# Kernel optimization log

Hardware: AMD Instinct MI355X
Metric: run time of the kernel (lower is better)

Reference implementation:

```python
import jax, jax.numpy as jnp
import numpy as np

B, S, DIM, H, DH, FF = 2, 2048, 2048, 16, 128, 8192
EPS = 1e-6


def rmsnorm(x, g):
    xf = x.astype(jnp.float32)
    y = xf * jax.lax.rsqrt(jnp.mean(xf * xf, axis=-1, keepdims=True) + EPS)
    return y.astype(x.dtype) * g


def rope_cache(seq_len, head_dim):
    inv_freq = 1.0 / (10000.0 ** (jnp.arange(0, head_dim, 2, dtype=jnp.float32) / head_dim))
    t = jnp.arange(seq_len, dtype=jnp.float32)
    freqs = jnp.outer(t, inv_freq)              # [S, DH/2]
    emb = jnp.concatenate([freqs, freqs], -1)   # [S, DH]
    return jnp.cos(emb), jnp.sin(emb)


def rotate_half(x):
    x1, x2 = jnp.split(x, 2, axis=-1)
    return jnp.concatenate([-x2, x1], axis=-1)


def apply_rope(x, cos, sin):
    # x: [B,H,S,DH]; cos/sin: [S,DH] broadcast per position
    c = cos[None, None, :, :]
    s = sin[None, None, :, :]
    return x * c + rotate_half(x) * s


def setup_inputs() -> dict:
    key = jax.random.key(0)
    ks = jax.random.split(key, 10)
    std = 0.02
    x = jax.random.normal(ks[0], (B, S, DIM), jnp.float32)
    mask = jnp.tril(jnp.ones((S, S), dtype=bool))[None, None]  # causal [1,1,S,S]
    wq = jax.random.normal(ks[1], (H * DH, DIM), jnp.float32) * std
    wk = jax.random.normal(ks[2], (H * DH, DIM), jnp.float32) * std
    wv = jax.random.normal(ks[3], (H * DH, DIM), jnp.float32) * std
    wo = jax.random.normal(ks[4], (DIM, H * DH), jnp.float32) * std
    w1 = jax.random.normal(ks[5], (FF, DIM), jnp.float32) * std
    w2 = jax.random.normal(ks[6], (DIM, FF), jnp.float32) * std
    w3 = jax.random.normal(ks[7], (FF, DIM), jnp.float32) * std
    g_attn = jnp.ones((DIM,), jnp.float32)
    g_ffn = jnp.ones((DIM,), jnp.float32)
    return {"x": x, "mask": mask, "wq": wq, "wk": wk, "wv": wv, "wo": wo,
            "w1": w1, "w2": w2, "w3": w3, "g_attn": g_attn, "g_ffn": g_ffn}


def reference(x, mask, wq, wk, wv, wo, w1, w2, w3, g_attn, g_ffn):
    b, s, _ = x.shape
    scale = 1.0 / np.sqrt(DH)
    # --- attention sublayer ---
    h = rmsnorm(x, g_attn)
    q = jnp.einsum('bsd,ed->bse', h, wq).reshape(b, s, H, DH).transpose(0, 2, 1, 3)
    k = jnp.einsum('bsd,ed->bse', h, wk).reshape(b, s, H, DH).transpose(0, 2, 1, 3)
    v = jnp.einsum('bsd,ed->bse', h, wv).reshape(b, s, H, DH).transpose(0, 2, 1, 3)
    cos, sin = rope_cache(s, DH)
    q = apply_rope(q, cos, sin)
    k = apply_rope(k, cos, sin)
    scores = jnp.einsum('bhqd,bhkd->bhqk', q, k) * scale
    scores = jnp.where(mask, scores, -1e9)
    attn = jax.nn.softmax(scores, axis=-1)
    o = jnp.einsum('bhqk,bhkd->bhqd', attn, v)
    o = o.transpose(0, 2, 1, 3).reshape(b, s, H * DH)
    x = x + jnp.einsum('bse,de->bsd', o, wo)
    # --- SwiGLU FFN sublayer ---
    h2 = rmsnorm(x, g_ffn)
    u = jnp.einsum('bsd,fd->bsf', h2, w1)
    g = jnp.einsum('bsd,fd->bsf', h2, w3)
    ff = jnp.einsum('bsf,df->bsd', jax.nn.silu(u) * g, w2)
    return x + ff
```

## Files before the change

### kernel.cpp

```cpp
#include <hip/hip_runtime.h>
#include <hip/hip_bf16.h>
#include <math.h>

typedef __hip_bfloat16 bf16;
typedef short short8 __attribute__((ext_vector_type(8)));
typedef float f32x4 __attribute__((ext_vector_type(4)));

#define Bq 2
#define Sq 2048
#define Dq 2048
#define Hq 16
#define DHq 128
#define FFq 8192
#define Mq 4096

__device__ __forceinline__ float b2f(bf16 x) { return __bfloat162float(x); }
__device__ __forceinline__ bf16 f2b(float x) { return __float2bfloat16(x); }

__device__ __forceinline__ void gload16(const void* g, void* lds_base) {
  __builtin_amdgcn_global_load_lds(
      (const __attribute__((address_space(1))) void*)g,
      (__attribute__((address_space(3))) void*)lds_base,
      16, 0, 0);
}

__global__ __launch_bounds__(256)
void conv_k(const float* __restrict__ src, bf16* __restrict__ dst, long n) {
  const long stride = (long)gridDim.x * 256 * 8;
  for (long i = ((long)blockIdx.x * 256 + threadIdx.x) * 8; i < n; i += stride) {
    f32x4 a = *(const f32x4*)(src + i);
    f32x4 b = *(const f32x4*)(src + i + 4);
    union { short8 s; bf16 h[8]; } u;
#pragma unroll
    for (int j = 0; j < 4; ++j) { u.h[j] = f2b(a[j]); u.h[j + 4] = f2b(b[j]); }
    *(short8*)(dst + i) = u.s;
  }
}

#define SB8()  __builtin_amdgcn_sched_barrier(0)
#define BAR8() { asm volatile("" ::: "memory"); __builtin_amdgcn_s_barrier(); asm volatile("" ::: "memory"); }
#define VMC4() { asm volatile("s_waitcnt vmcnt(4)" ::: "memory"); SB8(); }
#define LGK0() { asm volatile("s_waitcnt lgkmcnt(0)" ::: "memory"); SB8(); }

#define STG8(Gp, ldX, rowOff, kt, XsBuf)                                        \
  gload16(Gp + (size_t)((rowOff) + w8 + lr) * (size_t)(ldX) + (kt) + sCol,      \
          &XsBuf[(rowOff) + w8][0]);                                            \
  gload16(Gp + (size_t)((rowOff) + 64 + w8 + lr) * (size_t)(ldX) + (kt) + sCol, \
          &XsBuf[(rowOff) + 64 + w8][0]);

#define RD_A8(dst, XsBuf, mb)                                                   \
  _Pragma("unroll") for (int mi = 0; mi < 4; ++mi) {                            \
    const int ra = wmBase + ((mb) + mi) * 16 + c;                               \
    _Pragma("unroll") for (int kk = 0; kk < 2; ++kk)                            \
      dst[mi][kk] = *(const short8*)&XsBuf[ra][(((kk * 4 + g) ^ (ra & 7)) << 3)]; \
  }

#define RD_B8(dst, XsBuf, nb_)                                                  \
  _Pragma("unroll") for (int ni = 0; ni < 2; ++ni) {                            \
    const int rb = wnBase + ((nb_) + ni) * 16 + c;                              \
    _Pragma("unroll") for (int kk = 0; kk < 2; ++kk)                            \
      dst[ni][kk] = *(const short8*)&XsBuf[rb][(((kk * 4 + g) ^ (rb & 7)) << 3)]; \
  }

#define MFMA_Q8(afv, bfv, mb, nb_)                                              \
  __builtin_amdgcn_s_setprio(1);                                                \
  _Pragma("unroll") for (int mi = 0; mi < 4; ++mi)                              \
    _Pragma("unroll") for (int ni = 0; ni < 2; ++ni)                            \
      _Pragma("unroll") for (int kk = 0; kk < 2; ++kk)                          \
        acc[(mb) + mi][(nb_) + ni] = __builtin_amdgcn_mfma_f32_16x16x32_bf16(   \
            afv[mi][kk], bfv[ni][kk], acc[(mb) + mi][(nb_) + ni], 0, 0, 0);     \
  __builtin_amdgcn_s_setprio(0);

template <int EPI>
__global__ __launch_bounds__(512, 2)
void gemm8(const bf16* __restrict__ A, const bf16* __restrict__ Bt,
           const void* __restrict__ R, void* __restrict__ C,
           int N, int K, int ldb, long long boff) {
  __shared__ __align__(16) bf16 As[2][256][64];
  __shared__ __align__(16) bf16 Bs[2][256][64];
  const int tid = threadIdx.x;
  const int w = tid >> 6, l = tid & 63;
  const int g = l >> 4, c = l & 15;
  const int w8 = w * 8, lr = l >> 3;
  const int sCol = (((l & 7) ^ lr) << 3);

  const int nwg = gridDim.x * gridDim.y;
  const int orig = blockIdx.x + blockIdx.y * gridDim.x;
  const int qq = nwg >> 3, rr8 = nwg & 7;
  const int xcd = orig & 7, idx8 = orig >> 3;
  const int wg = (xcd < rr8 ? xcd * (qq + 1) : rr8 * (qq + 1) + (xcd - rr8) * qq) + idx8;
  const int bm = (wg / gridDim.x) * 256;
  const int bn = (wg % gridDim.x) * 256;

  const int wmBase = (w >> 2) * 128;
  const int wnBase = (w & 3) * 64;

  const bf16* Ab = A + (size_t)bm * K;
  const bf16* Bb = Bt + (size_t)bn * ldb + (size_t)boff;

  f32x4 acc[8][4] = {};
  const int nt = K >> 6;

  STG8(Ab, K, 0, 0, As[0]); STG8(Ab, K, 128, 0, As[0]);
  STG8(Bb, ldb, 0, 0, Bs[0]); STG8(Bb, ldb, 128, 0, Bs[0]);
  STG8(Bb, ldb, 0, 64, Bs[1]);
  STG8(Ab, K, 0, 64, As[1]);
  VMC4(); BAR8();

  short8 af[4][2], bf[2][2], af2[4][2], bf2[2][2];
  for (int it = 0; it < (nt >> 1); ++it) {
    const int t = it * 2;
    const int kt1 = (t + 1) << 6;
    const int kt2 = (t + 2 < nt ? t + 2 : nt - 1) << 6;
    const int kt3 = (t + 3 < nt ? t + 3 : nt - 1) << 6;
    RD_A8(af, As[0], 0); RD_B8(bf, Bs[0], 0);
    STG8(Ab, K, 128, kt1, As[1]);
    BAR8(); LGK0(); MFMA_Q8(af, bf, 0, 0); BAR8();
    RD_B8(bf2, Bs[0], 2);
    STG8(Bb, ldb, 128, kt1, Bs[1]);
    BAR8(); LGK0(); MFMA_Q8(af, bf2, 0, 2); BAR8();
    RD_A8(af2, As[0], 4);
    STG8(Bb, ldb, 0, kt2, Bs[0]);
    BAR8(); LGK0(); MFMA_Q8(af2, bf, 4, 0); BAR8();
    STG8(Ab, K, 0, kt2, As[0]);
    VMC4(); BAR8(); MFMA_Q8(af2, bf2, 4, 2); BAR8();
    RD_A8(af, As[1], 0); RD_B8(bf, Bs[1], 0);
    STG8(Ab, K, 128, kt2, As[0]);
    BAR8(); LGK0(); MFMA_Q8(af, bf, 0, 0); BAR8();
    RD_B8(bf2, Bs[1], 2);
    STG8(Bb, ldb, 128, kt2, Bs[0]);
    BAR8(); LGK0(); MFMA_Q8(af, bf2, 0, 2); BAR8();
    RD_A8(af2, As[1], 4);
    STG8(Bb, ldb, 0, kt3, Bs[1]);
    BAR8(); LGK0(); MFMA_Q8(af2, bf, 4, 0); BAR8();
    STG8(Ab, K, 0, kt3, As[1]);
    VMC4(); BAR8(); MFMA_Q8(af2, bf2, 4, 2); BAR8();
  }

  const int rbase = bm + wmBase + g * 4;
  const int cbase = bn + wnBase + c;
#pragma unroll
  for (int m = 0; m < 8; ++m)
#pragma unroll
    for (int r = 0; r < 4; ++r) {
      const int row = rbase + m * 16 + r;
#pragma unroll
      for (int n = 0; n < 4; ++n) {
        const size_t idx = (size_t)row * N + (cbase + n * 16);
        float vacc = acc[m][n][r];
        if (EPI == 1) {
          ((float*)C)[idx] = vacc + ((const float*)R)[idx];
        } else if (EPI == 2) {
          const float u = b2f(((const bf16*)R)[idx]);
          ((bf16*)C)[idx] = f2b((u / (1.f + expf(-u))) * vacc);
        } else {
          ((bf16*)C)[idx] = f2b(vacc);
        }
      }
    }
}

template <int EPI>
__global__ __launch_bounds__(256)
void gemm3(const bf16* __restrict__ A, const bf16* __restrict__ Bt,
           const void* __restrict__ R, void* __restrict__ C,
           int N, int K, int ldb, long long boff) {
  __shared__ __align__(16) bf16 As[128][64];
  __shared__ __align__(16) bf16 Bs[128][64];
  const int tid = threadIdx.x;
  const int w = tid >> 6;
  const int l = tid & 63;

  const int nwg = gridDim.x * gridDim.y;
  const int orig = blockIdx.x + blockIdx.y * gridDim.x;
  const int qq = nwg >> 3, rr8 = nwg & 7;
  const int xcd = orig & 7, idx8 = orig >> 3;
  const int wg = (xcd < rr8 ? xcd * (qq + 1) : rr8 * (qq + 1) + (xcd - rr8) * qq) + idx8;
  const int bm = (wg / gridDim.x) * 128;
  const int bn = (wg % gridDim.x) * 128;

  const int wr = (w >> 1) * 64;
  const int wc = (w & 1) * 64;
  f32x4 acc[4][4] = {};

  const bf16* Ab = A + (size_t)bm * K;
  const bf16* Bb = Bt + (size_t)bn * ldb + (size_t)boff;

  const int sRow = w * 8 + (l >> 3);
  const int sCol = (((l & 7) ^ (l >> 3)) << 3);

  for (int kt = 0; kt < K; kt += 64) {
    __syncthreads();
#pragma unroll
    for (int i = 0; i < 4; ++i) {
      gload16(Ab + (size_t)(i * 32 + sRow) * K + kt + sCol, &As[i * 32 + w * 8][0]);
      gload16(Bb + (size_t)(i * 32 + sRow) * ldb + kt + sCol, &Bs[i * 32 + w * 8][0]);
    }
    __syncthreads();

#pragma unroll
    for (int kk = 0; kk < 2; ++kk) {
      short8 af[4], bfv[4];
#pragma unroll
      for (int m = 0; m < 4; ++m) {
        const int ra = wr + m * 16 + (l & 15);
        af[m] = *(const short8*)&As[ra][(((kk * 4 + (l >> 4)) ^ (ra & 7)) << 3)];
      }
#pragma unroll
      for (int n = 0; n < 4; ++n) {
        const int rb = wc + n * 16 + (l & 15);
        bfv[n] = *(const short8*)&Bs[rb][(((kk * 4 + (l >> 4)) ^ (rb & 7)) << 3)];
      }
#pragma unroll
      for (int m = 0; m < 4; ++m)
#pragma unroll
        for (int n = 0; n < 4; ++n)
          acc[m][n] = __builtin_amdgcn_mfma_f32_16x16x32_bf16(af[m], bfv[n], acc[m][n], 0, 0, 0);
    }
  }

  const int rbase = bm + wr + (l >> 4) * 4;
  const int cbase = bn + wc + (l & 15);
#pragma unroll
  for (int m = 0; m < 4; ++m)
#pragma unroll
    for (int r = 0; r < 4; ++r) {
      const int row = rbase + m * 16 + r;
#pragma unroll
      for (int n = 0; n < 4; ++n) {
        const size_t idx = (size_t)row * N + (cbase + n * 16);
        float vacc = acc[m][n][r];
        if (EPI == 1) {
          ((float*)C)[idx] = vacc + ((const float*)R)[idx];
        } else if (EPI == 2) {
          const float u = b2f(((const bf16*)R)[idx]);
          ((bf16*)C)[idx] = f2b((u / (1.f + expf(-u))) * vacc);
        } else {
          ((bf16*)C)[idx] = f2b(vacc);
        }
      }
    }
}

template <int EPI>
__global__ __launch_bounds__(256)
void gemm2(const bf16* __restrict__ A, const float* __restrict__ Bt,
           const void* __restrict__ R, void* __restrict__ C,
           int N, int K, int ldb, long long boff) {
  __shared__ __align__(16) bf16 As[128][64];
  __shared__ __align__(16) float Bsf[128][64];
  const int tid = threadIdx.x;
  const int w = tid >> 6;
  const int l = tid & 63;

  const int nwg = gridDim.x * gridDim.y;
  const int orig = blockIdx.x + blockIdx.y * gridDim.x;
  const int qq = nwg >> 3, rr8 = nwg & 7;
  const int xcd = orig & 7, idx8 = orig >> 3;
  const int wg = (xcd < rr8 ? xcd * (qq + 1) : rr8 * (qq + 1) + (xcd - rr8) * qq) + idx8;
  const int bm = (wg / gridDim.x) * 128;
  const int bn = (wg % gridDim.x) * 128;

  const int wr = (w >> 1) * 64;
  const int wc = (w & 1) * 64;
  f32x4 acc[4][4] = {};

  const bf16* Ab = A + (size_t)bm * K;
  const float* Bb = Bt + (size_t)bn * ldb + (size_t)boff;

  const int aSrcCol = (((l & 7) ^ (l >> 3)) << 3);
  const int bKey = (w * 4 + (l >> 4)) & 7;
  const int bSrcCol = (((l & 15) ^ bKey) << 2);

  for (int kt = 0; kt < K; kt += 64) {
    __syncthreads();
#pragma unroll
    for (int i = 0; i < 4; ++i)
      gload16(Ab + (size_t)(i * 32 + w * 8 + (l >> 3)) * K + kt + aSrcCol,
              &As[i * 32 + w * 8][0]);
#pragma unroll
    for (int i = 0; i < 8; ++i)
      gload16(Bb + (size_t)(i * 16 + w * 4 + (l >> 4)) * ldb + kt + bSrcCol,
              &Bsf[i * 16 + w * 4][0]);
    __syncthreads();

#pragma unroll
    for (int kk = 0; kk < 2; ++kk) {
      short8 af[4], bfv[4];
#pragma unroll
      for (int m = 0; m < 4; ++m) {
        const int ra = wr + m * 16 + (l & 15);
        const int pb = (kk * 4 + (l >> 4)) ^ (ra & 7);
        af[m] = *(const short8*)&As[ra][pb * 8];
      }
#pragma unroll
      for (int n = 0; n < 4; ++n) {
        const int rb = wc + n * 16 + (l & 15);
        const int b0 = kk * 8 + (l >> 4) * 2;
        const f32x4 x0 = *(const f32x4*)&Bsf[rb][(b0 ^ (rb & 7)) * 4];
        const f32x4 x1 = *(const f32x4*)&Bsf[rb][((b0 + 1) ^ (rb & 7)) * 4];
        union { short8 s; bf16 h[8]; } u;
#pragma unroll
        for (int j = 0; j < 4; ++j) { u.h[j] = f2b(x0[j]); u.h[j + 4] = f2b(x1[j]); }
        bfv[n] = u.s;
      }
#pragma unroll
      for (int m = 0; m < 4; ++m)
#pragma unroll
        for (int n = 0; n < 4; ++n)
          acc[m][n] = __builtin_amdgcn_mfma_f32_16x16x32_bf16(af[m], bfv[n], acc[m][n], 0, 0, 0);
    }
  }

  const int rbase = bm + wr + (l >> 4) * 4;
  const int cbase = bn + wc + (l & 15);
#pragma unroll
  for (int m = 0; m < 4; ++m)
#pragma unroll
    for (int r = 0; r < 4; ++r) {
      const int row = rbase + m * 16 + r;
#pragma unroll
      for (int n = 0; n < 4; ++n) {
        const size_t idx = (size_t)row * N + (cbase + n * 16);
        float vacc = acc[m][n][r];
        if (EPI == 1) {
          ((float*)C)[idx] = vacc + ((const float*)R)[idx];
        } else if (EPI == 2) {
          const float u = b2f(((const bf16*)R)[idx]);
          ((bf16*)C)[idx] = f2b((u / (1.f + expf(-u))) * vacc);
        } else {
          ((bf16*)C)[idx] = f2b(vacc);
        }
      }
    }
}

__global__ __launch_bounds__(256)
void rmsnorm_k(const float* __restrict__ xin, const float* __restrict__ g,
               bf16* __restrict__ out) {
  const int row = blockIdx.x;
  const int tid = threadIdx.x;
  const float* xp = xin + (size_t)row * Dq + tid * 8;
  f32x4 a = *(const f32x4*)xp, b = *(const f32x4*)(xp + 4);
  float xf[8];
#pragma unroll
  for (int j = 0; j < 4; ++j) { xf[j] = a[j]; xf[j + 4] = b[j]; }
  float ss = 0.f;
#pragma unroll
  for (int j = 0; j < 8; ++j) ss += xf[j] * xf[j];
#pragma unroll
  for (int off = 32; off > 0; off >>= 1) ss += __shfl_down(ss, off);
  __shared__ float red[4];
  if ((tid & 63) == 0) red[tid >> 6] = ss;
  __syncthreads();
  const float rms = rsqrtf((red[0] + red[1] + red[2] + red[3]) * (1.f / (float)Dq) + 1e-6f);
  const float* gp = g + tid * 8;
  f32x4 ga = *(const f32x4*)gp, gb = *(const f32x4*)(gp + 4);
  union { short8 s; bf16 h[8]; } uo;
#pragma unroll
  for (int j = 0; j < 4; ++j) {
    uo.h[j] = f2b(xf[j] * rms * ga[j]);
    uo.h[j + 4] = f2b(xf[j + 4] * rms * gb[j]);
  }
  *(short8*)(out + (size_t)row * Dq + tid * 8) = uo.s;
}

__global__ __launch_bounds__(256)
void rope_k(bf16* __restrict__ q, bf16* __restrict__ k, int ld) {
  const size_t idx = (size_t)blockIdx.x * 256 + threadIdx.x;
  const int i = (int)(idx & 63);
  const int h = (int)((idx >> 6) & 15);
  const int s = (int)((idx >> 10) & 2047);
  const int b = (int)(idx >> 21);
  const float f = (float)s * powf(10000.f, -(float)i * (1.f / 64.f));
  float sn, cs;
  sincosf(f, &sn, &cs);
  const size_t base = ((size_t)(b * Sq + s)) * ld + h * DHq + i;
  const float qa = b2f(q[base]), qb_ = b2f(q[base + 64]);
  q[base] = f2b(qa * cs - qb_ * sn);
  q[base + 64] = f2b(qb_ * cs + qa * sn);
  const float ka = b2f(k[base]), kb_ = b2f(k[base + 64]);
  k[base] = f2b(ka * cs - kb_ * sn);
  k[base + 64] = f2b(kb_ * cs + ka * sn);
}

__device__ __forceinline__ int swz8(int row) { return (((row >> 3) ^ row) & 7) << 3; }

#define ATTN_COMPUTE(AQ, QB, QROW, M_, L_, OACC, KV0, CUR)                        \
  {                                                                               \
    f32x4 sc[4] = {};                                                             \
    __builtin_amdgcn_s_setprio(1);                                                \
    _Pragma("unroll") for (int n = 0; n < 4; ++n) {                               \
      const int krow = n * 16 + c;                                                \
      const int sw = swz8(krow);                                                  \
      _Pragma("unroll") for (int kk = 0; kk < 4; ++kk) {                          \
        short8 ak = *(const short8*)&Ks[CUR][krow][(kk * 32 + g * 8) ^ sw];       \
        sc[n] = __builtin_amdgcn_mfma_f32_16x16x32_bf16(ak, AQ[kk], sc[n], 0, 0, 0); \
      }                                                                           \
    }                                                                             \
    __builtin_amdgcn_s_setprio(0);                                                \
    float p[4][4];                                                                \
    float tmax = -3.0e38f;                                                        \
    if ((KV0) + 63 <= (QB)) {                                                     \
      _Pragma("unroll") for (int n = 0; n < 4; ++n)                               \
        _Pragma("unroll") for (int r = 0; r < 4; ++r) {                           \
          const float val = sc[n][r] * SCALE;                                     \
          p[n][r] = val;                                                          \
          tmax = fmaxf(tmax, val);                                                \
        }                                                                         \
    } else {                                                                      \
      _Pragma("unroll") for (int n = 0; n < 4; ++n)                               \
        _Pragma("unroll") for (int r = 0; r < 4; ++r) {                           \
          const int kvg = (KV0) + n * 16 + g * 4 + r;                             \
          float val = sc[n][r] * SCALE;                                           \
          if (kvg > (QROW)) val = -3.0e38f;                                       \
          p[n][r] = val;                                                          \
          tmax = fmaxf(tmax, val);                                                \
        }                                                                         \
    }                                                                             \
    tmax = fmaxf(tmax, __shfl_xor(tmax, 16));                                     \
    tmax = fmaxf(tmax, __shfl_xor(tmax, 32));                                     \
    const bool grow = !__all(tmax <= M_);                                         \
    const float m_new = grow ? fmaxf(M_, tmax) : M_;                              \
    float tsum = 0.f;                                                             \
    _Pragma("unroll") for (int n = 0; n < 4; ++n)                                 \
      _Pragma("unroll") for (int r = 0; r < 4; ++r) {                             \
        const float pv = expf(p[n][r] - m_new);                                   \
        p[n][r] = pv;                                                             \
        tsum += pv;                                                               \
      }                                                                           \
    tsum += __shfl_xor(tsum, 16);                                                 \
    tsum += __shfl_xor(tsum, 32);                                                 \
    if (grow) {                                                                   \
      const float corr = expf(M_ - m_new);                                        \
      L_ = L_ * corr + tsum;                                                      \
      M_ = m_new;                                                                 \
      _Pragma("unroll") for (int dt = 0; dt < 8; ++dt) OACC[dt] *= corr;          \
    } else {                                                                      \
      L_ += tsum;                                                                 \
    }                                                                             \
    const int keyc = (c ^ (c >> 3)) & 7;                                          \
    _Pragma("unroll") for (int n = 0; n < 4; ++n) {                               \
      union { unsigned long long u; bf16 hh[4]; } pk;                             \
      _Pragma("unroll") for (int r = 0; r < 4; ++r) pk.hh[r] = f2b(p[n][r]);      \
      const int blk = (2 * n + (g >> 1)) ^ keyc;                                  \
      *(unsigned long long*)&Ps[w][c][blk * 8 + (g & 1) * 4] = pk.u;              \
    }                                                                             \
    short8 ap[2];                                                                 \
    _Pragma("unroll") for (int kk = 0; kk < 2; ++kk)                              \
      ap[kk] = *(const short8*)&Ps[w][c][(kk * 32 + g * 8) ^ (keyc << 3)];        \
    __builtin_amdgcn_s_setprio(1);                                                \
    _Pragma("unroll") for (int dt = 0; dt < 8; ++dt) {                            \
      const int vrow = dt * 16 + c;                                               \
      const int vsw = swz8(vrow);                                                 \
      _Pragma("unroll") for (int kk = 0; kk < 2; ++kk) {                          \
        short8 av = *(const short8*)&Vt[CUR][vrow][(kk * 32 + g * 8) ^ vsw];      \
        OACC[dt] = __builtin_amdgcn_mfma_f32_16x16x32_bf16(av, ap[kk], OACC[dt], 0, 0, 0); \
      }                                                                           \
    }                                                                             \
    __builtin_amdgcn_s_setprio(0);                                                \
  }

__global__ __launch_bounds__(512)
void attn_k(const bf16* __restrict__ q, const bf16* __restrict__ k,
            const bf16* __restrict__ v, bf16* __restrict__ o, int ld) {
  __shared__ __align__(16) bf16 Ks[2][64][128];
  __shared__ __align__(16) bf16 Vt[2][128][64];
  __shared__ __align__(16) bf16 Ps[8][16][64];
  const int tid = threadIdx.x;
  const int w = tid >> 6, l = tid & 63;
  const int g = l >> 4, c = l & 15;
  const int x = blockIdx.x;
  const int h = blockIdx.y;
  const int b = blockIdx.z;
  const size_t hoff = (size_t)h * DHq;
  const float SCALE = 0.08838834764831845f;

  const int q0h = (15 - x) * 128, q0l = x * 128;
  const int qbh = q0h + w * 16, qbl = q0l + w * 16;
  const int qrh = qbh + c, qrl = qbl + c;

  short8 aqh[4], aql[4];
  {
    const bf16* qph = q + (size_t)(b * Sq + qrh) * ld + hoff + g * 8;
    const bf16* qpl = q + (size_t)(b * Sq + qrl) * ld + hoff + g * 8;
#pragma unroll
    for (int kk = 0; kk < 4; ++kk) {
      aqh[kk] = *(const short8*)(qph + kk * 32);
      aql[kk] = *(const short8*)(qpl + kk * 32);
    }
  }

  float mh = -3.0e38f, lh = 0.f, ml = -3.0e38f, ll_ = 0.f;
  f32x4 oh[8] = {}, ol[8] = {};

  const int stRow = tid >> 4;
  const int stBlk = tid & 15;
  const int ntiles = (q0h >> 6) + 2;

  {
#pragma unroll
    for (int i = 0; i < 2; ++i) {
      const int kr = i * 32 + w * 4 + (l >> 4);
      const int key = (kr ^ (kr >> 3)) & 7;
      gload16(k + (size_t)(b * Sq + kr) * ld + hoff + ((c ^ key) << 3),
              &Ks[0][i * 32 + w * 4][0]);
    }
    const int c0 = stBlk * 8;
#pragma unroll
    for (int i = 0; i < 2; ++i) {
      const int vr = i * 32 + stRow;
      union { short8 s; bf16 hh[8]; } uv;
      uv.s = *(const short8*)(v + (size_t)(b * Sq + vr) * ld + hoff + c0);
#pragma unroll
      for (int j = 0; j < 8; ++j) Vt[0][c0 + j][vr ^ swz8(c0 + j)] = uv.hh[j];
    }
  }
  __syncthreads();

  for (int t = 0; t < ntiles; ++t) {
    const int cur = t & 1, nxt = cur ^ 1;
    const int kv0 = t * 64;
    const bool pf = (t + 1 < ntiles);
    short8 vpa, vpb;
    if (pf) {
      const int kvn = kv0 + 64;
#pragma unroll
      for (int i = 0; i < 2; ++i) {
        const int kr = i * 32 + w * 4 + (l >> 4);
        const int key = (kr ^ (kr >> 3)) & 7;
        gload16(k + (size_t)(b * Sq + kvn + kr) * ld + hoff + ((c ^ key) << 3),
                &Ks[nxt][i * 32 + w * 4][0]);
      }
      vpa = *(const short8*)(v + (size_t)(b * Sq + kvn + stRow) * ld + hoff + stBlk * 8);
      vpb = *(const short8*)(v + (size_t)(b * Sq + kvn + 32 + stRow) * ld + hoff + stBlk * 8);
    }

    if (kv0 <= qbh + 15) ATTN_COMPUTE(aqh, qbh, qrh, mh, lh, oh, kv0, cur);

    if (pf) {
      const int c0 = stBlk * 8;
      union { short8 s; bf16 hh[8]; } uv;
      uv.s = vpa;
#pragma unroll
      for (int j = 0; j < 8; ++j) Vt[nxt][c0 + j][stRow ^ swz8(c0 + j)] = uv.hh[j];
      uv.s = vpb;
#pragma unroll
      for (int j = 0; j < 8; ++j) Vt[nxt][c0 + j][(32 + stRow) ^ swz8(c0 + j)] = uv.hh[j];
    }

    if (kv0 <= qbl + 15) ATTN_COMPUTE(aql, qbl, qrl, ml, ll_, ol, kv0, cur);

    __syncthreads();
  }

  {
    const float inv = 1.f / lh;
    bf16* op = o + (size_t)(b * Sq + qrh) * Dq + hoff + g * 4;
#pragma unroll
    for (int dt = 0; dt < 8; ++dt) {
      union { unsigned long long u; bf16 hh[4]; } pk;
#pragma unroll
      for (int r = 0; r < 4; ++r) pk.hh[r] = f2b(oh[dt][r] * inv);
      *(unsigned long long*)(op + dt * 16) = pk.u;
    }
  }
  {
    const float inv = 1.f / ll_;
    bf16* op = o + (size_t)(b * Sq + qrl) * Dq + hoff + g * 4;
#pragma unroll
    for (int dt = 0; dt < 8; ++dt) {
      union { unsigned long long u; bf16 hh[4]; } pk;
#pragma unroll
      for (int r = 0; r < 4; ++r) pk.hh[r] = f2b(ol[dt][r] * inv);
      *(unsigned long long*)(op + dt * 16) = pk.u;
    }
  }
}

extern "C" void kernel_launch(void* const* d_in, const int* in_sizes, int n_in,
                              void* d_out, int out_size, void* d_ws, size_t ws_size,
                              hipStream_t stream) {
  (void)in_sizes; (void)n_in; (void)out_size;
  const float* x  = (const float*)d_in[0];
  const float* wq = (const float*)d_in[2];
  const float* wk = (const float*)d_in[3];
  const float* wv = (const float*)d_in[4];
  const float* wo = (const float*)d_in[5];
  const float* w1 = (const float*)d_in[6];
  const float* w2 = (const float*)d_in[7];
  const float* w3 = (const float*)d_in[8];
  const float* ga = (const float*)d_in[9];
  const float* gf = (const float*)d_in[10];
  float* out = (float*)d_out;

  char* ws = (char*)d_ws;
  dim3 blk(256);
  dim3 gA(8, Hq, Bq);
  dim3 blkA(512);
  dim3 blk8(512);

  const size_t SZ_H   = (size_t)Mq * Dq * 2;
  const size_t SZ_QKV = (size_t)Mq * 3 * Dq * 2;
  const size_t SZ_W4  = (size_t)Dq * Dq * 2;
  const size_t SZ_W13 = (size_t)FFq * Dq * 2;
  const size_t ACT    = SZ_H + SZ_QKV;
  const size_t WTS    = 3 * SZ_W4 + SZ_W4 + 3 * SZ_W13;
  const size_t NEED   = ACT + WTS;

  if (ws_size >= NEED) {
    bf16* h    = (bf16*)(ws);
    bf16* qkv  = (bf16*)(ws + SZ_H);
    bf16* ob   = h;
    bf16* h2   = qkv;
    bf16* ub   = (bf16*)(ws + SZ_H + SZ_H);
    char* wb   = ws + ACT;
    bf16* wqkv_b = (bf16*)(wb);
    bf16* wo_b   = (bf16*)(wb + 3 * SZ_W4);
    bf16* w1_b   = (bf16*)(wb + 4 * SZ_W4);
    bf16* w3_b   = (bf16*)(wb + 4 * SZ_W4 + SZ_W13);
    bf16* w2_b   = (bf16*)(wb + 4 * SZ_W4 + 2 * SZ_W13);

    const long nW4 = (long)Dq * Dq, nW13 = (long)FFq * Dq;
    conv_k<<<1024, blk, 0, stream>>>(wq, wqkv_b, nW4);
    conv_k<<<1024, blk, 0, stream>>>(wk, wqkv_b + nW4, nW4);
    conv_k<<<1024, blk, 0, stream>>>(wv, wqkv_b + 2 * nW4, nW4);
    conv_k<<<1024, blk, 0, stream>>>(wo, wo_b, nW4);
    conv_k<<<2048, blk, 0, stream>>>(w1, w1_b, nW13);
    conv_k<<<2048, blk, 0, stream>>>(w3, w3_b, nW13);
    conv_k<<<2048, blk, 0, stream>>>(w2, w2_b, nW13);

    rmsnorm_k<<<Mq, blk, 0, stream>>>(x, ga, h);
    gemm8<0><<<dim3(24, 16), blk8, 0, stream>>>(h, wqkv_b, nullptr, qkv, 6144, Dq, Dq, 0);
    rope_k<<<(Bq * Sq * Hq * 64) / 256, blk, 0, stream>>>(qkv, qkv + Dq, 3 * Dq);
    attn_k<<<gA, blkA, 0, stream>>>(qkv, qkv + Dq, qkv + 2 * Dq, ob, 3 * Dq);
    gemm8<1><<<dim3(8, 16), blk8, 0, stream>>>(ob, wo_b, x, out, Dq, Dq, Dq, 0);
    rmsnorm_k<<<Mq, blk, 0, stream>>>(out, gf, h2);
    for (int hh = 0; hh < 2; ++hh) {
      bf16* w1h = w1_b + (size_t)hh * 4096 * Dq;
      bf16* w3h = w3_b + (size_t)hh * 4096 * Dq;
      gemm8<0><<<dim3(16, 16), blk8, 0, stream>>>(h2, w1h, nullptr, ub, 4096, Dq, Dq, 0);
      gemm8<2><<<dim3(16, 16), blk8, 0, stream>>>(h2, w3h, ub, ub, 4096, Dq, Dq, 0);
      gemm3<1><<<dim3(16, 32), blk, 0, stream>>>(ub, w2_b, out, out, Dq, 4096, FFq,
                                                 (long long)hh * 4096);
    }
  } else {
    const size_t MS = (size_t)Mq * Dq * 2;
    bf16* h  = (bf16*)(ws);
    bf16* kb = (bf16*)(ws + MS);
    bf16* vb = (bf16*)(ws + 2 * MS);
    bf16* qb = (bf16*)(ws + 3 * MS);
    bf16* ub = (bf16*)(ws);
    bf16* ob = h;
    bf16* h2 = qb;

    dim3 gD(Dq / 128, Mq / 128);
    dim3 gU(32, Mq / 128);

    rmsnorm_k<<<Mq, blk, 0, stream>>>(x, ga, h);
    gemm2<0><<<gD, blk, 0, stream>>>(h, wq, nullptr, qb, Dq, Dq, Dq, 0);
    gemm2<0><<<gD, blk, 0, stream>>>(h, wk, nullptr, kb, Dq, Dq, Dq, 0);
    gemm2<0><<<gD, blk, 0, stream>>>(h, wv, nullptr, vb, Dq, Dq, Dq, 0);
    rope_k<<<(Bq * Sq * Hq * 64) / 256, blk, 0, stream>>>(qb, kb, Dq);
    attn_k<<<gA, blkA, 0, stream>>>(qb, kb, vb, ob, Dq);
    gemm2<1><<<gD, blk, 0, stream>>>(ob, wo, x, out, Dq, Dq, Dq, 0);
    rmsnorm_k<<<Mq, blk, 0, stream>>>(out, gf, h2);
    for (int hh = 0; hh < 2; ++hh) {
      const long long bo13 = (long long)hh * 4096 * 2048;
      gemm2<0><<<gU, blk, 0, stream>>>(h2, w1, nullptr, ub, 4096, Dq, Dq, bo13);
      gemm2<2><<<gU, blk, 0, stream>>>(h2, w3, ub, ub, 4096, Dq, Dq, bo13);
      gemm2<1><<<gD, blk, 0, stream>>>(ub, w2, out, out, Dq, 4096, FFq,
                                       (long long)hh * 4096);
    }
  }
}
```

Measured before the change: 930.6 us.

## Restructure gemm8 pipeline into coarser stages and route QKV/Wo GEMMs to gemm3

Reorganizes the 256x256 gemm8 main loop so each half-tile stage loads all A or B rows at once and issues two MFMA quads per barrier pair. It drops the explicit lgkmcnt(0) waits and sched barriers and leaves LDS read ordering to the compiler, which is meant to cut barrier and wait overhead. The QKV and output projection GEMMs are also switched from gemm8 to the smaller-tile gemm3 kernel with larger grids, likely for better occupancy and CU coverage on those shapes. The gemm8 prologue no longer preloads the first A tile for stage 1, and the removed LDS waits may break read-before-overwrite ordering.

Result: faster. 891.9 us (-4.2%).

```diff
diff --git a/kernel.cpp b/kernel.cpp
--- a/kernel.cpp
+++ b/kernel.cpp
@@ -37,10 +37,8 @@
   }
 }
 
-#define SB8()  __builtin_amdgcn_sched_barrier(0)
 #define BAR8() { asm volatile("" ::: "memory"); __builtin_amdgcn_s_barrier(); asm volatile("" ::: "memory"); }
-#define VMC4() { asm volatile("s_waitcnt vmcnt(4)" ::: "memory"); SB8(); }
-#define LGK0() { asm volatile("s_waitcnt lgkmcnt(0)" ::: "memory"); SB8(); }
+#define VMC4() { asm volatile("s_waitcnt vmcnt(4)" ::: "memory"); __builtin_amdgcn_sched_barrier(0); }
 
 #define STG8(Gp, ldX, rowOff, kt, XsBuf)                                        \
   gload16(Gp + (size_t)((rowOff) + w8 + lr) * (size_t)(ldX) + (kt) + sCol,      \
@@ -103,38 +101,35 @@
 
   STG8(Ab, K, 0, 0, As[0]); STG8(Ab, K, 128, 0, As[0]);
   STG8(Bb, ldb, 0, 0, Bs[0]); STG8(Bb, ldb, 128, 0, Bs[0]);
-  STG8(Bb, ldb, 0, 64, Bs[1]);
-  STG8(Ab, K, 0, 64, As[1]);
+  STG8(Bb, ldb, 0, 64, Bs[1]); STG8(Bb, ldb, 128, 64, Bs[1]);
   VMC4(); BAR8();
 
-  short8 af[4][2], bf[2][2], af2[4][2], bf2[2][2];
+  short8 af[4][2], af2[4][2], bf[2][2], bf2[2][2];
   for (int it = 0; it < (nt >> 1); ++it) {
     const int t = it * 2;
     const int kt1 = (t + 1) << 6;
     const int kt2 = (t + 2 < nt ? t + 2 : nt - 1) << 6;
     const int kt3 = (t + 3 < nt ? t + 3 : nt - 1) << 6;
-    RD_A8(af, As[0], 0); RD_B8(bf, Bs[0], 0);
-    STG8(Ab, K, 128, kt1, As[1]);
-    BAR8(); LGK0(); MFMA_Q8(af, bf, 0, 0); BAR8();
-    RD_B8(bf2, Bs[0], 2);
-    STG8(Bb, ldb, 128, kt1, Bs[1]);
-    BAR8(); LGK0(); MFMA_Q8(af, bf2, 0, 2); BAR8();
+    RD_A8(af, As[0], 0); RD_B8(bf, Bs[0], 0); RD_B8(bf2, Bs[0], 2);
+    STG8(Ab, K, 0, kt1, As[1]); STG8(Ab, K, 128, kt1, As[1]);
+    BAR8();
+    MFMA_Q8(af, bf, 0, 0); MFMA_Q8(af, bf2, 0, 2);
+    BAR8();
     RD_A8(af2, As[0], 4);
-    STG8(Bb, ldb, 0, kt2, Bs[0]);
-    BAR8(); LGK0(); MFMA_Q8(af2, bf, 4, 0); BAR8();
-    STG8(Ab, K, 0, kt2, As[0]);
-    VMC4(); BAR8(); MFMA_Q8(af2, bf2, 4, 2); BAR8();
-    RD_A8(af, As[1], 0); RD_B8(bf, Bs[1], 0);
-    STG8(Ab, K, 128, kt2, As[0]);
-    BAR8(); LGK0(); MFMA_Q8(af, bf, 0, 0); BAR8();
-    RD_B8(bf2, Bs[1], 2);
-    STG8(Bb, ldb, 128, kt2, Bs[0]);
-    BAR8(); LGK0(); MFMA_Q8(af, bf2, 0, 2); BAR8();
+    STG8(Bb, ldb, 0, kt2, Bs[0]); STG8(Bb, ldb, 128, kt2, Bs[0]);
+    BAR8();
+    MFMA_Q8(af2, bf, 4, 0); MFMA_Q8(af2, bf2, 4, 2);
+    VMC4(); BAR8();
+    RD_A8(af, As[1], 0); RD_B8(bf, Bs[1], 0); RD_B8(bf2, Bs[1], 2);
+    STG8(Ab, K, 0, kt2, As[0]); STG8(Ab, K, 128, kt2, As[0]);
+    BAR8();
+    MFMA_Q8(af, bf, 0, 0); MFMA_Q8(af, bf2, 0, 2);
+    BAR8();
     RD_A8(af2, As[1], 4);
-    STG8(Bb, ldb, 0, kt3, Bs[1]);
-    BAR8(); LGK0(); MFMA_Q8(af2, bf, 4, 0); BAR8();
-    STG8(Ab, K, 0, kt3, As[1]);
-    VMC4(); BAR8(); MFMA_Q8(af2, bf2, 4, 2); BAR8();
+    STG8(Bb, ldb, 0, kt3, Bs[1]); STG8(Bb, ldb, 128, kt3, Bs[1]);
+    BAR8();
+    MFMA_Q8(af2, bf, 4, 0); MFMA_Q8(af2, bf2, 4, 2);
+    VMC4(); BAR8();
   }
 
   const int rbase = bm + wmBase + g * 4;
@@ -631,10 +626,10 @@
     conv_k<<<2048, blk, 0, stream>>>(w2, w2_b, nW13);
 
     rmsnorm_k<<<Mq, blk, 0, stream>>>(x, ga, h);
-    gemm8<0><<<dim3(24, 16), blk8, 0, stream>>>(h, wqkv_b, nullptr, qkv, 6144, Dq, Dq, 0);
+    gemm3<0><<<dim3(48, 32), blk, 0, stream>>>(h, wqkv_b, nullptr, qkv, 6144, Dq, Dq, 0);
     rope_k<<<(Bq * Sq * Hq * 64) / 256, blk, 0, stream>>>(qkv, qkv + Dq, 3 * Dq);
     attn_k<<<gA, blkA, 0, stream>>>(qkv, qkv + Dq, qkv + 2 * Dq, ob, 3 * Dq);
-    gemm8<1><<<dim3(8, 16), blk8, 0, stream>>>(ob, wo_b, x, out, Dq, Dq, Dq, 0);
+    gemm3<1><<<dim3(16, 32), blk, 0, stream>>>(ob, wo_b, x, out, Dq, Dq, Dq, 0);
     rmsnorm_k<<<Mq, blk, 0, stream>>>(out, gf, h2);
     for (int hh = 0; hh < 2; ++hh) {
       bf16* w1h = w1_b + (size_t)hh * 4096 * Dq;
```
